# Performance work log

Measured on AMD Instinct MI355X. Metric: run time of the kernel, lower is better.

Reference implementation:

```python
import jax, jax.numpy as jnp
import numpy as np

N_NODES = 100000
N_EDGES = 1600000
IN_DIM = 128
HID = 256
N_CLS = 32
BN_EPS = 1e-5


def _sage_conv(x, src, dst, Wl, bl, Wr, n_nodes):
    # PyG SAGEConv (mean aggr): out = lin_l(mean_{j->i} x_j) + lin_r(x_i)
    msgs = x[src]                                              # [E, D] gather
    agg = jax.ops.segment_sum(msgs, dst, num_segments=n_nodes)  # [N, D]
    deg = jax.ops.segment_sum(jnp.ones((src.shape[0],), x.dtype), dst,
                              num_segments=n_nodes)
    agg = agg / jnp.maximum(deg, 1.0)[:, None]                 # mean
    return agg @ Wl + bl + x @ Wr


def _batch_norm(x, gamma, beta):
    mu = jnp.mean(x, axis=0)
    var = jnp.var(x, axis=0)
    return (x - mu) * jax.lax.rsqrt(var + BN_EPS) * gamma + beta


def setup_inputs() -> dict:
    key = jax.random.key(0)
    ks = jax.random.split(key, 8)
    s = lambda d: 1.0 / np.sqrt(d)
    return {
        "x": jax.random.normal(ks[0], (N_NODES, IN_DIM), jnp.float32),
        "edge_src": jax.random.randint(ks[1], (N_EDGES,), 0, N_NODES),
        "edge_dst": jax.random.randint(ks[2], (N_EDGES,), 0, N_NODES),
        "W1l": jax.random.normal(ks[3], (IN_DIM, HID), jnp.float32) * s(IN_DIM),
        "b1": jnp.zeros((HID,), jnp.float32),
        "W1r": jax.random.normal(ks[4], (IN_DIM, HID), jnp.float32) * s(IN_DIM),
        "g1": jnp.ones((HID,), jnp.float32),
        "be1": jnp.zeros((HID,), jnp.float32),
        "W2l": jax.random.normal(ks[5], (HID, HID), jnp.float32) * s(HID),
        "b2": jnp.zeros((HID,), jnp.float32),
        "W2r": jax.random.normal(ks[6], (HID, HID), jnp.float32) * s(HID),
        "g2": jnp.ones((HID,), jnp.float32),
        "be2": jnp.zeros((HID,), jnp.float32),
        "Wfc": jax.random.normal(ks[7], (HID, N_CLS), jnp.float32) * s(HID),
        "bfc": jnp.zeros((N_CLS,), jnp.float32),
    }


def reference(x, edge_src, edge_dst, W1l, b1, W1r, g1, be1,
              W2l, b2, W2r, g2, be2, Wfc, bfc):
    n = x.shape[0]
    h = _sage_conv(x, edge_src, edge_dst, W1l, b1, W1r, n)
    h = jax.nn.relu(_batch_norm(h, g1, be1))
    # dropout is identity in deterministic/eval mode
    h = _sage_conv(h, edge_src, edge_dst, W2l, b2, W2r, n)
    h = jax.nn.relu(_batch_norm(h, g2, be2))
    return h @ Wfc + bfc
```

## Files before the change

### kernel.cpp

```cpp
#include <hip/hip_runtime.h>

#define N_NODES 100000
#define N_EDGES 1600000
#define IN_DIM 128
#define HID 256
#define N_CLS 32
#define BN_EPS 1e-5f

#define SCAN_CHUNK 1024
#define SCAN_NB ((N_NODES + SCAN_CHUNK - 1) / SCAN_CHUNK)
#define GEMM_NBY ((N_NODES + 127) / 128)
#define GEMM_NB (GEMM_NBY * 2)

#define NBUCK 16
#define BUCK_NODES 6250
#define BUCK_CAP 112000
#define PASSA_CHUNK 2048
#define PASSA_NB ((N_EDGES + PASSA_CHUNK - 1) / PASSA_CHUNK)
#define HSUBS 32

typedef unsigned short bf16;
typedef __attribute__((ext_vector_type(8))) short short8;
typedef __attribute__((ext_vector_type(4))) float float4v;
typedef __attribute__((ext_vector_type(2))) float floatx2;

__device__ __forceinline__ float bf2f(bf16 h) {
    return __uint_as_float(((unsigned int)h) << 16);
}
__device__ __forceinline__ bf16 f2bf(float f) {
    unsigned int u = __float_as_uint(f);
    u += 0x7FFFu + ((u >> 16) & 1u);
    return (bf16)(u >> 16);
}
__device__ __forceinline__ float blo(unsigned int u) { return __uint_as_float(u << 16); }
__device__ __forceinline__ float bhi(unsigned int u) { return __uint_as_float(u & 0xFFFF0000u); }
__device__ __forceinline__ unsigned int pack2(float lo, float hi) {
    return (unsigned int)f2bf(lo) | ((unsigned int)f2bf(hi) << 16);
}

__device__ __forceinline__ void acc16_fp8(uint4 w, floatx2* a) {
    a[0] += __builtin_amdgcn_cvt_pk_f32_fp8(w.x, false);
    a[1] += __builtin_amdgcn_cvt_pk_f32_fp8(w.x, true);
    a[2] += __builtin_amdgcn_cvt_pk_f32_fp8(w.y, false);
    a[3] += __builtin_amdgcn_cvt_pk_f32_fp8(w.y, true);
    a[4] += __builtin_amdgcn_cvt_pk_f32_fp8(w.z, false);
    a[5] += __builtin_amdgcn_cvt_pk_f32_fp8(w.z, true);
    a[6] += __builtin_amdgcn_cvt_pk_f32_fp8(w.w, false);
    a[7] += __builtin_amdgcn_cvt_pk_f32_fp8(w.w, true);
}
__device__ __forceinline__ unsigned int pack4_fp8(float a, float b, float c, float d) {
    int p = 0;
    p = __builtin_amdgcn_cvt_pk_fp8_f32(a, b, p, false);
    p = __builtin_amdgcn_cvt_pk_fp8_f32(c, d, p, true);
    return (unsigned int)p;
}

__device__ __forceinline__ void gload16(const void* g, void* l) {
    __builtin_amdgcn_global_load_lds(
        (const __attribute__((address_space(1))) void*)g,
        (__attribute__((address_space(3))) void*)l, 16, 0, 0);
}


__global__ __launch_bounds__(256) void bucket_scatter_kernel(
    const int* __restrict__ esrc, const int* __restrict__ edst,
    int* __restrict__ bcur, int2* __restrict__ bstore) {
    __shared__ int lhist[NBUCK], lbase[NBUCK], gbase[NBUCK], lcur[NBUCK];
    __shared__ int2 stage[PASSA_CHUNK];
    const int tid = threadIdx.x;
    if (tid < NBUCK) lhist[tid] = 0;
    __syncthreads();

    const int base = blockIdx.x * PASSA_CHUNK;
    const int nedge = min(PASSA_CHUNK, N_EDGES - base);
    const bool act = (tid * 8) < nedge;
    int s[8], d[8], bk[8];
    if (act) {
        const int4* s4 = (const int4*)(esrc + base + tid * 8);
        const int4* d4 = (const int4*)(edst + base + tid * 8);
#pragma unroll
        for (int t = 0; t < 2; ++t) {
            int4 sv = s4[t], dv = d4[t];
            s[t * 4 + 0] = sv.x; s[t * 4 + 1] = sv.y; s[t * 4 + 2] = sv.z; s[t * 4 + 3] = sv.w;
            d[t * 4 + 0] = dv.x; d[t * 4 + 1] = dv.y; d[t * 4 + 2] = dv.z; d[t * 4 + 3] = dv.w;
        }
#pragma unroll
        for (int u = 0; u < 8; ++u) {
            bk[u] = (int)((unsigned)d[u] / BUCK_NODES);
            atomicAdd(&lhist[bk[u]], 1);
        }
    }
    __syncthreads();
    if (tid == 0) {
        int run = 0;
#pragma unroll
        for (int b = 0; b < NBUCK; ++b) { lbase[b] = run; lcur[b] = run; run += lhist[b]; }
    }
    if (tid < NBUCK) gbase[tid] = atomicAdd(&bcur[tid], lhist[tid]);
    __syncthreads();
    if (act) {
#pragma unroll
        for (int u = 0; u < 8; ++u) {
            int p = atomicAdd(&lcur[bk[u]], 1);
            stage[p] = make_int2(s[u], d[u]);
        }
    }
    __syncthreads();
    for (int p = tid; p < nedge; p += 256) {
        int2 e = stage[p];
        int b = (int)((unsigned)e.y / BUCK_NODES);
        int gp = gbase[b] + (p - lbase[b]);
        if (gp < BUCK_CAP) bstore[(size_t)b * BUCK_CAP + gp] = e;
    }
}


__global__ __launch_bounds__(256) void bucket_hist_kernel(
    const int2* __restrict__ bstore, const int* __restrict__ bcnt,
    int* __restrict__ partial) {
    __shared__ int hist[BUCK_NODES];
    const int bk = blockIdx.x & (NBUCK - 1);
    const int sl = blockIdx.x >> 4;
    for (int i = threadIdx.x; i < BUCK_NODES; i += 256) hist[i] = 0;
    __syncthreads();
    const int n = bcnt[bk];
    const int per = (n + HSUBS - 1) / HSUBS;
    const int i0 = sl * per, i1 = min(i0 + per, n);
    const int2* ep = bstore + (size_t)bk * BUCK_CAP;
    const int nbase = bk * BUCK_NODES;
    for (int i = i0 + threadIdx.x; i < i1; i += 256) {
        atomicAdd(&hist[ep[i].y - nbase], 1);
    }
    __syncthreads();
    int* dst = partial + (size_t)sl * N_NODES + nbase;
    for (int i = threadIdx.x; i < BUCK_NODES; i += 256) dst[i] = hist[i];
}


__global__ __launch_bounds__(256) void fill_bucket_kernel(
    const int2* __restrict__ bstore, const int* __restrict__ bcnt,
    const int* __restrict__ off, const int* __restrict__ partial,
    int* __restrict__ csr) {
    __shared__ int basec[BUCK_NODES];
    const int bk = blockIdx.x & (NBUCK - 1);
    const int sl = blockIdx.x >> 4;
    const int nbase = bk * BUCK_NODES;
    const int* prow = partial + (size_t)sl * N_NODES + nbase;
    const int* orow = off + nbase;
    for (int i = threadIdx.x; i < BUCK_NODES; i += 256) basec[i] = orow[i] + prow[i];
    __syncthreads();
    const int n = bcnt[bk];
    const int per = (n + HSUBS - 1) / HSUBS;
    const int i0 = sl * per, i1 = min(i0 + per, n);
    const int2* ep = bstore + (size_t)bk * BUCK_CAP;
    for (int i = i0 + threadIdx.x; i < i1; i += 256) {
        int2 e = ep[i];
        int p = atomicAdd(&basec[e.y - nbase], 1);
        csr[p] = e.x;
    }
}


__global__ void scan1_kernel(int* __restrict__ partial, int* __restrict__ counts,
                             int* __restrict__ bsums) {
    __shared__ int wsum[4];
    int base = blockIdx.x * SCAN_CHUNK + threadIdx.x * 4;
    int c0 = 0, c1 = 0, c2 = 0, c3 = 0;
    if (base + 4 <= N_NODES) {
#pragma unroll
        for (int sl = 0; sl < HSUBS; ++sl) {
            int* p = partial + (size_t)sl * N_NODES + base;
            int4 v = *(const int4*)p;
            int4 w; w.x = c0; w.y = c1; w.z = c2; w.w = c3;
            *(int4*)p = w;
            c0 += v.x; c1 += v.y; c2 += v.z; c3 += v.w;
        }
        int4 w; w.x = c0; w.y = c1; w.z = c2; w.w = c3;
        *(int4*)(counts + base) = w;
    } else {
        for (int j = 0; j < 4; ++j) {
            if (base + j < N_NODES) {
                int c = 0;
                for (int sl = 0; sl < HSUBS; ++sl) {
                    int* p = partial + (size_t)sl * N_NODES + base + j;
                    int v = *p; *p = c; c += v;
                }
                counts[base + j] = c;
                if (j == 0) c0 = c; else if (j == 1) c1 = c; else if (j == 2) c2 = c; else c3 = c;
            }
        }
    }
    int s = c0 + c1 + c2 + c3;
    for (int d = 32; d > 0; d >>= 1) s += __shfl_down(s, d, 64);
    if ((threadIdx.x & 63) == 0) wsum[threadIdx.x >> 6] = s;
    __syncthreads();
    if (threadIdx.x == 0) bsums[blockIdx.x] = wsum[0] + wsum[1] + wsum[2] + wsum[3];
}

__global__ void scan2_kernel(const int* __restrict__ bsums, int* __restrict__ boffs) {
    __shared__ int sh[128];
    int i = threadIdx.x;
    int v = (i < SCAN_NB) ? bsums[i] : 0;
    sh[i] = v;
    __syncthreads();
    for (int d = 1; d < 128; d <<= 1) {
        int t = (i >= d) ? sh[i - d] : 0;
        __syncthreads();
        sh[i] += t;
        __syncthreads();
    }
    if (i < SCAN_NB) boffs[i] = sh[i] - v;
}

__global__ void scan3_kernel(const int* __restrict__ counts, const int* __restrict__ boffs,
                             int* __restrict__ off) {
    __shared__ int sh[256];
    int tid = threadIdx.x;
    int base = blockIdx.x * SCAN_CHUNK + tid * 4;
    int c0 = 0, c1 = 0, c2 = 0, c3 = 0;
    if (base + 4 <= N_NODES) {
        int4 v = *(const int4*)(counts + base);
        c0 = v.x; c1 = v.y; c2 = v.z; c3 = v.w;
    } else {
        if (base + 0 < N_NODES) c0 = counts[base + 0];
        if (base + 1 < N_NODES) c1 = counts[base + 1];
        if (base + 2 < N_NODES) c2 = counts[base + 2];
        if (base + 3 < N_NODES) c3 = counts[base + 3];
    }
    int ts = c0 + c1 + c2 + c3;
    sh[tid] = ts;
    __syncthreads();
    for (int d = 1; d < 256; d <<= 1) {
        int t = (tid >= d) ? sh[tid - d] : 0;
        __syncthreads();
        sh[tid] += t;
        __syncthreads();
    }
    int run = boffs[blockIdx.x] + sh[tid] - ts;
    if (base + 0 < N_NODES) off[base + 0] = run; run += c0;
    if (base + 1 < N_NODES) off[base + 1] = run; run += c1;
    if (base + 2 < N_NODES) off[base + 2] = run; run += c2;
    if (base + 3 < N_NODES) off[base + 3] = run;
    if (blockIdx.x == 0 && tid == 0) off[N_NODES] = N_EDGES;
}


__global__ void convert_x_kernel(const float* __restrict__ x, bf16* __restrict__ xb,
                                 unsigned char* __restrict__ xf8) {
    int i = blockIdx.x * blockDim.x + threadIdx.x;
    int total4 = N_NODES * IN_DIM / 4;
    if (i >= total4) return;
    float4 v = ((const float4*)x)[i];
    ushort4 r;
    r.x = f2bf(v.x); r.y = f2bf(v.y); r.z = f2bf(v.z); r.w = f2bf(v.w);
    ((ushort4*)xb)[i] = r;
    ((unsigned int*)xf8)[i] = pack4_fp8(v.x, v.y, v.z, v.w);
}


__global__ void prep_weights_kernel(const float* __restrict__ W1l, const float* __restrict__ W1r,
                                    const float* __restrict__ W2l, const float* __restrict__ W2r,
                                    const float* __restrict__ Wfc,
                                    bf16* __restrict__ w1lt, bf16* __restrict__ w1rt,
                                    bf16* __restrict__ w2lt, bf16* __restrict__ w2rt,
                                    bf16* __restrict__ wfct) {
    const int S1 = IN_DIM * HID;
    const int S2 = HID * HID;
    const int S3 = HID * N_CLS;
    int i = blockIdx.x * blockDim.x + threadIdx.x;
    if (i < 2 * S1 + 2 * S2) {
        const float* W; bf16* Wt; int K, idx;
        if (i < S1)          { W = W1l; Wt = w1lt; K = IN_DIM; idx = i; }
        else if (i < 2 * S1) { W = W1r; Wt = w1rt; K = IN_DIM; idx = i - S1; }
        else if (i < 2 * S1 + S2) { W = W2l; Wt = w2lt; K = HID; idx = i - 2 * S1; }
        else                 { W = W2r; Wt = w2rt; K = HID; idx = i - 2 * S1 - S2; }
        int k = idx / HID, n = idx - k * HID;
        Wt[(size_t)n * K + k] = f2bf(W[idx]);
    } else if (i < 2 * S1 + 2 * S2 + S3) {
        int idx = i - 2 * S1 - 2 * S2;
        int k = idx >> 5, n = idx & 31;
        wfct[(size_t)n * HID + k] = f2bf(Wfc[idx]);
    }
}


__global__ __launch_bounds__(256) void aggregate1_kernel(
    const unsigned char* __restrict__ xf8, const int* __restrict__ off,
    const int* __restrict__ csr, bf16* __restrict__ out) {
    int t = blockIdx.x * blockDim.x + threadIdx.x;
    int node = t >> 3;
    int sl = t & 7;
    if (node >= N_NODES) return;
    int s = off[node], e = off[node + 1];
    float inv = 1.0f / (float)max(e - s, 1);
    const uint4* f = (const uint4*)xf8;
    floatx2 a[8];
#pragma unroll
    for (int k = 0; k < 8; ++k) a[k] = (floatx2){0.f, 0.f};
    int i = s;
    for (; i + 8 <= e; i += 8) {
        uint4 w[8];
#pragma unroll
        for (int u = 0; u < 8; ++u) w[u] = f[csr[i + u] * 8 + sl];
#pragma unroll
        for (int u = 0; u < 8; ++u) acc16_fp8(w[u], a);
    }
    for (; i + 4 <= e; i += 4) {
        uint4 w[4];
#pragma unroll
        for (int u = 0; u < 4; ++u) w[u] = f[csr[i + u] * 8 + sl];
#pragma unroll
        for (int u = 0; u < 4; ++u) acc16_fp8(w[u], a);
    }
    for (; i < e; ++i) acc16_fp8(f[csr[i] * 8 + sl], a);
    uint4 r0, r1;
    r0.x = pack2(a[0].x * inv, a[0].y * inv);
    r0.y = pack2(a[1].x * inv, a[1].y * inv);
    r0.z = pack2(a[2].x * inv, a[2].y * inv);
    r0.w = pack2(a[3].x * inv, a[3].y * inv);
    r1.x = pack2(a[4].x * inv, a[4].y * inv);
    r1.y = pack2(a[5].x * inv, a[5].y * inv);
    r1.z = pack2(a[6].x * inv, a[6].y * inv);
    r1.w = pack2(a[7].x * inv, a[7].y * inv);
    ((uint4*)out)[node * 16 + sl * 2] = r0;
    ((uint4*)out)[node * 16 + sl * 2 + 1] = r1;
}

__global__ __launch_bounds__(256) void aggregate2_kernel(
    const unsigned char* __restrict__ hf8, const int* __restrict__ off,
    const int* __restrict__ csr, bf16* __restrict__ out) {
    int t = blockIdx.x * blockDim.x + threadIdx.x;
    int node = t >> 4;
    int sl = t & 15;
    if (node >= N_NODES) return;
    int s = off[node], e = off[node + 1];
    float inv = 1.0f / (float)max(e - s, 1);
    const uint4* f = (const uint4*)hf8;
    floatx2 a[8];
#pragma unroll
    for (int k = 0; k < 8; ++k) a[k] = (floatx2){0.f, 0.f};
    int i = s;
    for (; i + 8 <= e; i += 8) {
        uint4 w[8];
#pragma unroll
        for (int u = 0; u < 8; ++u) w[u] = f[csr[i + u] * 16 + sl];
#pragma unroll
        for (int u = 0; u < 8; ++u) acc16_fp8(w[u], a);
    }
    for (; i + 4 <= e; i += 4) {
        uint4 w[4];
#pragma unroll
        for (int u = 0; u < 4; ++u) w[u] = f[csr[i + u] * 16 + sl];
#pragma unroll
        for (int u = 0; u < 4; ++u) acc16_fp8(w[u], a);
    }
    for (; i < e; ++i) acc16_fp8(f[csr[i] * 16 + sl], a);
    uint4 r0, r1;
    r0.x = pack2(a[0].x * inv, a[0].y * inv);
    r0.y = pack2(a[1].x * inv, a[1].y * inv);
    r0.z = pack2(a[2].x * inv, a[2].y * inv);
    r0.w = pack2(a[3].x * inv, a[3].y * inv);
    r1.x = pack2(a[4].x * inv, a[4].y * inv);
    r1.y = pack2(a[5].x * inv, a[5].y * inv);
    r1.z = pack2(a[6].x * inv, a[6].y * inv);
    r1.w = pack2(a[7].x * inv, a[7].y * inv);
    ((uint4*)out)[node * 32 + sl * 2] = r0;
    ((uint4*)out)[node * 32 + sl * 2 + 1] = r1;
}


#define AT_SZ 4096

__device__ __forceinline__ void stage_tile(
    const bf16* __restrict__ Ap, const bf16* __restrict__ Wp, int K, int k0,
    int tile_m, int tile_n, int M, int wave, int lane,
    bf16* bufA, bf16* bufW) {
#pragma unroll
    for (int is = 0; is < 2; ++is) {
        int lin = (wave * 2 + is) * 1024 + lane * 16;
        int row = lin >> 6;
        int seg = (lin >> 4) & 3;
        int ga = min(tile_m + row, M - 1);
        gload16(Ap + (size_t)ga * K + k0 + seg * 8, (char*)bufA + (wave * 2 + is) * 1024);
        gload16(Wp + (size_t)(tile_n + row) * K + k0 + seg * 8, (char*)bufW + (wave * 2 + is) * 1024);
    }
}

__global__ __launch_bounds__(256) void gemm_dual_mfma(
    const bf16* __restrict__ A, const bf16* __restrict__ WtA, int KA,
    const bf16* __restrict__ Bm, const bf16* __restrict__ WtB, int KB,
    const float* __restrict__ bias, bf16* __restrict__ C, int M,
    float* __restrict__ psum, float* __restrict__ psq) {
    __shared__ bf16 As[3 * AT_SZ];
    __shared__ bf16 Ws[3 * AT_SZ];
    __shared__ float sred[4][64];
    __shared__ float qred[4][64];
    const int tid = threadIdx.x;
    const int lane = tid & 63;
    const int wave = tid >> 6;
    const int rw = (wave >> 1) * 64;
    const int cw = (wave & 1) * 64;
    const int lrow = lane & 15;
    const int quad = lane >> 4;
    const int tile_m = blockIdx.y * 128;
    const int tile_n = blockIdx.x * 128;

    float4v acc[4][4];
#pragma unroll
    for (int i = 0; i < 4; ++i)
#pragma unroll
        for (int j = 0; j < 4; ++j) acc[i][j] = (float4v){0.f, 0.f, 0.f, 0.f};

    const int NTA = KA >> 5;
    const int NT = NTA + (KB >> 5);
    auto tsrc = [&](int t, const bf16*& Ap, const bf16*& Wp, int& K, int& k0) {
        if (t < NTA) { Ap = A;  Wp = WtA; K = KA; k0 = t << 5; }
        else         { Ap = Bm; Wp = WtB; K = KB; k0 = (t - NTA) << 5; }
    };

#pragma unroll
    for (int t = 0; t < 2; ++t) {
        const bf16 *Ap, *Wp; int K, k0; tsrc(t, Ap, Wp, K, k0);
        stage_tile(Ap, Wp, K, k0, tile_m, tile_n, M, wave, lane,
                   As + t * AT_SZ, Ws + t * AT_SZ);
    }

    for (int t = 0; t < NT; ++t) {
        if (t + 2 < NT) {
            const bf16 *Ap, *Wp; int K, k0; tsrc(t + 2, Ap, Wp, K, k0);
            int b = (t + 2) % 3;
            stage_tile(Ap, Wp, K, k0, tile_m, tile_n, M, wave, lane,
                       As + b * AT_SZ, Ws + b * AT_SZ);
        }
        if (t + 2 < NT)      asm volatile("s_waitcnt vmcnt(8)" ::: "memory");
        else if (t + 1 < NT) asm volatile("s_waitcnt vmcnt(4)" ::: "memory");
        else                 asm volatile("s_waitcnt vmcnt(0)" ::: "memory");
        __builtin_amdgcn_s_barrier();
        asm volatile("" ::: "memory");

        const bf16* bA = As + (t % 3) * AT_SZ;
        const bf16* bW = Ws + (t % 3) * AT_SZ;
        short8 a[4], b[4];
#pragma unroll
        for (int i = 0; i < 4; ++i)
            a[i] = *(const short8*)(bA + (rw + i * 16 + lrow) * 32 + quad * 8);
#pragma unroll
        for (int j = 0; j < 4; ++j)
            b[j] = *(const short8*)(bW + (cw + j * 16 + lrow) * 32 + quad * 8);
#pragma unroll
        for (int i = 0; i < 4; ++i)
#pragma unroll
            for (int j = 0; j < 4; ++j)
                acc[i][j] = __builtin_amdgcn_mfma_f32_16x16x32_bf16(a[i], b[j], acc[i][j], 0, 0, 0);

        asm volatile("" ::: "memory");
        __builtin_amdgcn_s_barrier();
    }

    bf16* slice = As + wave * 1024;
    float bvj[4];
#pragma unroll
    for (int j = 0; j < 4; ++j) bvj[j] = bias[tile_n + cw + j * 16 + lrow];
    float cs[4] = {0.f, 0.f, 0.f, 0.f}, cq[4] = {0.f, 0.f, 0.f, 0.f};

#pragma unroll
    for (int i = 0; i < 4; ++i) {
#pragma unroll
        for (int j = 0; j < 4; ++j) {
#pragma unroll
            for (int r = 0; r < 4; ++r) {
                int row = tile_m + rw + i * 16 + quad * 4 + r;
                float v = acc[i][j][r] + bvj[j];
                if (row < M) { cs[j] += v; cq[j] += v * v; }
                slice[(quad * 4 + r) * 64 + ((j ^ quad) * 16) + lrow] = f2bf(v);
            }
        }
        __syncthreads();
#pragma unroll
        for (int c = 0; c < 2; ++c) {
            int ch = lane + c * 64;
            int lr = ch >> 3, sg = ch & 7;
            int grow = tile_m + rw + i * 16 + lr;
            if (grow < M) {
                const bf16* srcp = slice + lr * 64 + (((sg >> 1) ^ (lr >> 2)) << 4) + ((sg & 1) << 3);
                uint4 v = *(const uint4*)srcp;
                *(uint4*)(C + (size_t)grow * HID + tile_n + cw + sg * 8) = v;
            }
        }
        __syncthreads();
    }

#pragma unroll
    for (int j = 0; j < 4; ++j) {
        cs[j] += __shfl_xor(cs[j], 16, 64); cs[j] += __shfl_xor(cs[j], 32, 64);
        cq[j] += __shfl_xor(cq[j], 16, 64); cq[j] += __shfl_xor(cq[j], 32, 64);
    }
    if (quad == 0) {
#pragma unroll
        for (int j = 0; j < 4; ++j) {
            sred[wave][j * 16 + lrow] = cs[j];
            qred[wave][j * 16 + lrow] = cq[j];
        }
    }
    __syncthreads();
    int bid = blockIdx.y * gridDim.x + blockIdx.x;
    if (tid < 128) {
        int grp = tid >> 6, idx = tid & 63;
        psum[(size_t)bid * 128 + tid] = sred[grp][idx] + sred[grp + 2][idx];
    } else {
        int t = tid - 128;
        int grp = t >> 6, idx = t & 63;
        psq[(size_t)bid * 128 + t] = qred[grp][idx] + qred[grp + 2][idx];
    }
}

__global__ void bn_finalize_kernel(const float* __restrict__ psum, const float* __restrict__ psq,
                                   float* __restrict__ stats, int nby) {
    const float* src = blockIdx.y ? psq : psum;
    int c = threadIdx.x;
    int bx = c >> 7, cl = c & 127;
    int per = (nby + gridDim.x - 1) / gridDim.x;
    int b0 = blockIdx.x * per, b1 = min(b0 + per, nby);
    float s = 0.f;
    for (int by = b0; by < b1; ++by) s += src[(size_t)(by * 2 + bx) * 128 + cl];
    atomicAdd(&stats[blockIdx.y * HID + c], s);
}


__global__ void bn_apply_relu_kernel(bf16* __restrict__ h, unsigned char* __restrict__ hf8,
                                     const float* __restrict__ stats,
                                     const float* __restrict__ g, const float* __restrict__ be,
                                     int M) {
    int i4 = blockIdx.x * blockDim.x + threadIdx.x;
    int total4 = M * (HID / 4);
    if (i4 >= total4) return;
    int col4 = i4 & (HID / 4 - 1);
    ushort4 v = ((const ushort4*)h)[i4];
    float invN = 1.0f / (float)M;
    float o[4] = {bf2f(v.x), bf2f(v.y), bf2f(v.z), bf2f(v.w)};
#pragma unroll
    for (int j = 0; j < 4; ++j) {
        int col = col4 * 4 + j;
        float mu = stats[col] * invN;
        float var = stats[HID + col] * invN - mu * mu;
        float sc = rsqrtf(var + BN_EPS) * g[col];
        float val = (o[j] - mu) * sc + be[col];
        o[j] = val > 0.f ? val : 0.f;
    }
    ushort4 r;
    r.x = f2bf(o[0]); r.y = f2bf(o[1]); r.z = f2bf(o[2]); r.w = f2bf(o[3]);
    ((ushort4*)h)[i4] = r;
    ((unsigned int*)hf8)[i4] = pack4_fp8(o[0], o[1], o[2], o[3]);
}


#define BSTR 264

__global__ __launch_bounds__(256) void fc_bn_mfma_kernel(
    const bf16* __restrict__ h, const float* __restrict__ stats,
    const float* __restrict__ g, const float* __restrict__ be,
    const bf16* __restrict__ WfcT, const float* __restrict__ bfc,
    float* __restrict__ out, int M) {
    __shared__ bf16 Bs[32 * BSTR];
    __shared__ float sc_s[HID], sh_s[HID];
    int tid = threadIdx.x;
    for (int i = tid; i < 32 * 32; i += 256) {
        int rrow = i >> 5, seg = i & 31;
        *(uint4*)(Bs + rrow * BSTR + seg * 8) = *(const uint4*)(WfcT + (size_t)rrow * HID + seg * 8);
    }
    {
        float invN = 1.0f / (float)M;
        float mu = stats[tid] * invN;
        float var = stats[HID + tid] * invN - mu * mu;
        float s = rsqrtf(var + BN_EPS) * g[tid];
        sc_s[tid] = s;
        sh_s[tid] = be[tid] - mu * s;
    }
    __syncthreads();
    int wave = tid >> 6, lane = tid & 63, lrow = lane & 15, quad = lane >> 4;
    int row = blockIdx.x * 64 + wave * 16 + lrow;
    const bf16* hrow = h + (size_t)row * HID;
    float4v acc0 = {0.f, 0.f, 0.f, 0.f}, acc1 = {0.f, 0.f, 0.f, 0.f};
#pragma unroll
    for (int ks = 0; ks < 8; ++ks) {
        int k0 = ks * 32 + quad * 8;
        uint4 av = {0u, 0u, 0u, 0u};
        if (row < M) av = *(const uint4*)(hrow + k0);
        union { unsigned int u[4]; short8 s8; } cvt;
        unsigned int* avp = (unsigned int*)&av;
#pragma unroll
        for (int t = 0; t < 4; ++t) {
            int k = k0 + t * 2;
            float v0 = blo(avp[t]) * sc_s[k] + sh_s[k];
            float v1 = bhi(avp[t]) * sc_s[k + 1] + sh_s[k + 1];
            v0 = v0 > 0.f ? v0 : 0.f;
            v1 = v1 > 0.f ? v1 : 0.f;
            cvt.u[t] = pack2(v0, v1);
        }
        short8 b0 = *(const short8*)(Bs + lrow * BSTR + k0);
        short8 b1 = *(const short8*)(Bs + (16 + lrow) * BSTR + k0);
        acc0 = __builtin_amdgcn_mfma_f32_16x16x32_bf16(cvt.s8, b0, acc0, 0, 0, 0);
        acc1 = __builtin_amdgcn_mfma_f32_16x16x32_bf16(cvt.s8, b1, acc1, 0, 0, 0);
    }
    int orow = blockIdx.x * 64 + wave * 16 + quad * 4;
    float bv0 = bfc[lrow], bv1 = bfc[16 + lrow];
#pragma unroll
    for (int r = 0; r < 4; ++r) {
        int rr = orow + r;
        if (rr < M) {
            out[(size_t)rr * N_CLS + lrow] = acc0[r] + bv0;
            out[(size_t)rr * N_CLS + 16 + lrow] = acc1[r] + bv1;
        }
    }
}


extern "C" void kernel_launch(void* const* d_in, const int* in_sizes, int n_in,
                              void* d_out, int out_size, void* d_ws, size_t ws_size,
                              hipStream_t stream) {
    const float* x   = (const float*)d_in[0];
    const int* esrc  = (const int*)d_in[1];
    const int* edst  = (const int*)d_in[2];
    const float* W1l = (const float*)d_in[3];
    const float* b1  = (const float*)d_in[4];
    const float* W1r = (const float*)d_in[5];
    const float* g1  = (const float*)d_in[6];
    const float* be1 = (const float*)d_in[7];
    const float* W2l = (const float*)d_in[8];
    const float* b2  = (const float*)d_in[9];
    const float* W2r = (const float*)d_in[10];
    const float* g2  = (const float*)d_in[11];
    const float* be2 = (const float*)d_in[12];
    const float* Wfc = (const float*)d_in[13];
    const float* bfc = (const float*)d_in[14];
    float* out = (float*)d_out;

    char* ws = (char*)d_ws;
    size_t o = 0;
    auto carve = [&](size_t bytes) {
        char* p = ws + o;
        o = (o + bytes + 255) & ~(size_t)255;
        return p;
    };
    int*   off    = (int*)carve((N_NODES + 1) * sizeof(int));
    int*   cursor = (int*)carve(N_NODES * sizeof(int));
    int*   csr    = (int*)carve(N_EDGES * sizeof(int));
    int*   bsums  = (int*)carve(SCAN_NB * sizeof(int));
    int*   boffs  = (int*)carve(SCAN_NB * sizeof(int));
    int*   bcur   = (int*)carve(NBUCK * sizeof(int));
    float* stats1 = (float*)carve(2 * HID * sizeof(float));
    float* stats2 = (float*)carve(2 * HID * sizeof(float));
    float* psum   = (float*)carve((size_t)GEMM_NB * 128 * sizeof(float));
    float* psq    = (float*)carve((size_t)GEMM_NB * 128 * sizeof(float));
    bf16*  w1lt   = (bf16*)carve((size_t)IN_DIM * HID * sizeof(bf16));
    bf16*  w1rt   = (bf16*)carve((size_t)IN_DIM * HID * sizeof(bf16));
    bf16*  w2lt   = (bf16*)carve((size_t)HID * HID * sizeof(bf16));
    bf16*  w2rt   = (bf16*)carve((size_t)HID * HID * sizeof(bf16));
    bf16*  wfct   = (bf16*)carve((size_t)N_CLS * HID * sizeof(bf16));
    bf16*  agg    = (bf16*)carve((size_t)N_NODES * HID * sizeof(bf16));
    bf16*  h1     = (bf16*)carve((size_t)N_NODES * HID * sizeof(bf16));
    bf16*  h2     = (bf16*)carve((size_t)N_NODES * HID * sizeof(bf16));
    bf16*          xb   = h2;
    unsigned char* xf8  = (unsigned char*)h2 + (size_t)N_NODES * IN_DIM * sizeof(bf16);
    unsigned char* h1f8 = (unsigned char*)h2;
    int2*          bstore = (int2*)agg;
    int*           partial = (int*)h1;

    if (o > ws_size) return;

    hipMemsetAsync(bcur, 0, NBUCK * sizeof(int), stream);
    hipMemsetAsync(stats1, 0, 2 * HID * sizeof(float), stream);
    hipMemsetAsync(stats2, 0, 2 * HID * sizeof(float), stream);

    bucket_scatter_kernel<<<PASSA_NB, 256, 0, stream>>>(esrc, edst, bcur, bstore);
    bucket_hist_kernel<<<NBUCK * HSUBS, 256, 0, stream>>>(bstore, bcur, partial);
    scan1_kernel<<<SCAN_NB, 256, 0, stream>>>(partial, cursor, bsums);
    scan2_kernel<<<1, 128, 0, stream>>>(bsums, boffs);
    scan3_kernel<<<SCAN_NB, 256, 0, stream>>>(cursor, boffs, off);
    fill_bucket_kernel<<<NBUCK * HSUBS, 256, 0, stream>>>(bstore, bcur, off, partial, csr);

    convert_x_kernel<<<(N_NODES * IN_DIM / 4 + 255) / 256, 256, 0, stream>>>(x, xb, xf8);
    {
        int total = 2 * IN_DIM * HID + 2 * HID * HID + HID * N_CLS;
        prep_weights_kernel<<<(total + 255) / 256, 256, 0, stream>>>(
            W1l, W1r, W2l, W2r, Wfc, w1lt, w1rt, w2lt, w2rt, wfct);
    }

    const dim3 ggrid(HID / 128, GEMM_NBY);

    aggregate1_kernel<<<(N_NODES * 8 + 255) / 256, 256, 0, stream>>>(xf8, off, csr, agg);
    gemm_dual_mfma<<<ggrid, 256, 0, stream>>>(
        agg, w1lt, IN_DIM, xb, w1rt, IN_DIM, b1, h1, N_NODES, psum, psq);
    bn_finalize_kernel<<<dim3(8, 2), 256, 0, stream>>>(psum, psq, stats1, GEMM_NBY);
    {
        int total4 = N_NODES * (HID / 4);
        bn_apply_relu_kernel<<<(total4 + 255) / 256, 256, 0, stream>>>(h1, h1f8, stats1, g1, be1, N_NODES);
    }

    aggregate2_kernel<<<(N_NODES * 16 + 255) / 256, 256, 0, stream>>>(h1f8, off, csr, agg);
    gemm_dual_mfma<<<ggrid, 256, 0, stream>>>(
        agg, w2lt, HID, h1, w2rt, HID, b2, h2, N_NODES, psum, psq);
    bn_finalize_kernel<<<dim3(8, 2), 256, 0, stream>>>(psum, psq, stats2, GEMM_NBY);

    fc_bn_mfma_kernel<<<(N_NODES + 63) / 64, 256, 0, stream>>>(
        h2, stats2, g2, be2, wfct, bfc, out, N_NODES);
}
```

Before: 454.1 us.

## Remap aggregation threads to feature slices across blocks, add nontemporal csr/output access

Aggregation kernels now assign each block one 32-byte feature slice for a range of nodes, two threads per node, with adjacent block IDs covering different slices of the same nodes. Previously all slices of a node were handled by consecutive threads of one wavefront. The aim is to narrow the gather working set per block so it fits cache better, and to keep concurrent blocks touching nearby rows. The csr index loads and the aggregated output stores are made nontemporal so they do not evict cached feature rows. In exchange, each block reads csr and offsets separately for every slice, repeating index traffic and divergent degree loops.

```diff
diff --git a/kernel.cpp b/kernel.cpp
--- a/kernel.cpp
+++ b/kernel.cpp
@@ -23,6 +23,7 @@
 typedef __attribute__((ext_vector_type(8))) short short8;
 typedef __attribute__((ext_vector_type(4))) float float4v;
 typedef __attribute__((ext_vector_type(2))) float floatx2;
+typedef __attribute__((ext_vector_type(4))) unsigned int uint4v;
 
 __device__ __forceinline__ float bf2f(bf16 h) {
     return __uint_as_float(((unsigned int)h) << 16);
@@ -287,13 +288,15 @@
 __global__ __launch_bounds__(256) void aggregate1_kernel(
     const unsigned char* __restrict__ xf8, const int* __restrict__ off,
     const int* __restrict__ csr, bf16* __restrict__ out) {
-    int t = blockIdx.x * blockDim.x + threadIdx.x;
-    int node = t >> 3;
-    int sl = t & 7;
+    const int key = blockIdx.x & 7;
+    const int slice = key >> 1;
+    const int node = (blockIdx.x >> 3) * 256 + (key & 1) * 128 + (threadIdx.x >> 1);
+    const int half = threadIdx.x & 1;
     if (node >= N_NODES) return;
     int s = off[node], e = off[node + 1];
     float inv = 1.0f / (float)max(e - s, 1);
     const uint4* f = (const uint4*)xf8;
+    const int boff = slice * 2 + half;
     floatx2 a[8];
 #pragma unroll
     for (int k = 0; k < 8; ++k) a[k] = (floatx2){0.f, 0.f};
@@ -301,19 +304,19 @@
     for (; i + 8 <= e; i += 8) {
         uint4 w[8];
 #pragma unroll
-        for (int u = 0; u < 8; ++u) w[u] = f[csr[i + u] * 8 + sl];
+        for (int u = 0; u < 8; ++u) w[u] = f[__builtin_nontemporal_load(csr + i + u) * 8 + boff];
 #pragma unroll
         for (int u = 0; u < 8; ++u) acc16_fp8(w[u], a);
     }
     for (; i + 4 <= e; i += 4) {
         uint4 w[4];
 #pragma unroll
-        for (int u = 0; u < 4; ++u) w[u] = f[csr[i + u] * 8 + sl];
+        for (int u = 0; u < 4; ++u) w[u] = f[__builtin_nontemporal_load(csr + i + u) * 8 + boff];
 #pragma unroll
         for (int u = 0; u < 4; ++u) acc16_fp8(w[u], a);
     }
-    for (; i < e; ++i) acc16_fp8(f[csr[i] * 8 + sl], a);
-    uint4 r0, r1;
+    for (; i < e; ++i) acc16_fp8(f[__builtin_nontemporal_load(csr + i) * 8 + boff], a);
+    uint4v r0, r1;
     r0.x = pack2(a[0].x * inv, a[0].y * inv);
     r0.y = pack2(a[1].x * inv, a[1].y * inv);
     r0.z = pack2(a[2].x * inv, a[2].y * inv);
@@ -322,20 +325,22 @@
     r1.y = pack2(a[5].x * inv, a[5].y * inv);
     r1.z = pack2(a[6].x * inv, a[6].y * inv);
     r1.w = pack2(a[7].x * inv, a[7].y * inv);
-    ((uint4*)out)[node * 16 + sl * 2] = r0;
-    ((uint4*)out)[node * 16 + sl * 2 + 1] = r1;
+    uint4v* dst = (uint4v*)out + node * 16 + slice * 4 + half * 2;
+    __builtin_nontemporal_store(r0, dst);
+    __builtin_nontemporal_store(r1, dst + 1);
 }
 
 __global__ __launch_bounds__(256) void aggregate2_kernel(
     const unsigned char* __restrict__ hf8, const int* __restrict__ off,
     const int* __restrict__ csr, bf16* __restrict__ out) {
-    int t = blockIdx.x * blockDim.x + threadIdx.x;
-    int node = t >> 4;
-    int sl = t & 15;
+    const int slice = blockIdx.x & 7;
+    const int node = (blockIdx.x >> 3) * 128 + (threadIdx.x >> 1);
+    const int half = threadIdx.x & 1;
     if (node >= N_NODES) return;
     int s = off[node], e = off[node + 1];
     float inv = 1.0f / (float)max(e - s, 1);
     const uint4* f = (const uint4*)hf8;
+    const int boff = slice * 2 + half;
     floatx2 a[8];
 #pragma unroll
     for (int k = 0; k < 8; ++k) a[k] = (floatx2){0.f, 0.f};
@@ -343,19 +348,19 @@
     for (; i + 8 <= e; i += 8) {
         uint4 w[8];
 #pragma unroll
-        for (int u = 0; u < 8; ++u) w[u] = f[csr[i + u] * 16 + sl];
+        for (int u = 0; u < 8; ++u) w[u] = f[__builtin_nontemporal_load(csr + i + u) * 16 + boff];
 #pragma unroll
         for (int u = 0; u < 8; ++u) acc16_fp8(w[u], a);
     }
     for (; i + 4 <= e; i += 4) {
         uint4 w[4];
 #pragma unroll
-        for (int u = 0; u < 4; ++u) w[u] = f[csr[i + u] * 16 + sl];
+        for (int u = 0; u < 4; ++u) w[u] = f[__builtin_nontemporal_load(csr + i + u) * 16 + boff];
 #pragma unroll
         for (int u = 0; u < 4; ++u) acc16_fp8(w[u], a);
     }
-    for (; i < e; ++i) acc16_fp8(f[csr[i] * 16 + sl], a);
-    uint4 r0, r1;
+    for (; i < e; ++i) acc16_fp8(f[__builtin_nontemporal_load(csr + i) * 16 + boff], a);
+    uint4v r0, r1;
     r0.x = pack2(a[0].x * inv, a[0].y * inv);
     r0.y = pack2(a[1].x * inv, a[1].y * inv);
     r0.z = pack2(a[2].x * inv, a[2].y * inv);
@@ -364,8 +369,9 @@
     r1.y = pack2(a[5].x * inv, a[5].y * inv);
     r1.z = pack2(a[6].x * inv, a[6].y * inv);
     r1.w = pack2(a[7].x * inv, a[7].y * inv);
-    ((uint4*)out)[node * 32 + sl * 2] = r0;
-    ((uint4*)out)[node * 32 + sl * 2 + 1] = r1;
+    uint4v* dst = (uint4v*)out + node * 32 + slice * 4 + half * 2;
+    __builtin_nontemporal_store(r0, dst);
+    __builtin_nontemporal_store(r1, dst + 1);
 }
 
 
@@ -688,7 +694,7 @@
 
     const dim3 ggrid(HID / 128, GEMM_NBY);
 
-    aggregate1_kernel<<<(N_NODES * 8 + 255) / 256, 256, 0, stream>>>(xf8, off, csr, agg);
+    aggregate1_kernel<<<8 * ((N_NODES + 255) / 256), 256, 0, stream>>>(xf8, off, csr, agg);
     gemm_dual_mfma<<<ggrid, 256, 0, stream>>>(
         agg, w1lt, IN_DIM, xb, w1rt, IN_DIM, b1, h1, N_NODES, psum, psq);
     bn_finalize_kernel<<<dim3(8, 2), 256, 0, stream>>>(psum, psq, stats1, GEMM_NBY);
@@ -697,7 +703,7 @@
         bn_apply_relu_kernel<<<(total4 + 255) / 256, 256, 0, stream>>>(h1, h1f8, stats1, g1, be1, N_NODES);
     }
 
-    aggregate2_kernel<<<(N_NODES * 16 + 255) / 256, 256, 0, stream>>>(h1f8, off, csr, agg);
+    aggregate2_kernel<<<8 * ((N_NODES + 127) / 128), 256, 0, stream>>>(h1f8, off, csr, agg);
     gemm_dual_mfma<<<ggrid, 256, 0, stream>>>(
         agg, w2lt, HID, h1, w2rt, HID, b2, h2, N_NODES, psum, psq);
     bn_finalize_kernel<<<dim3(8, 2), 256, 0, stream>>>(psum, psq, stats2, GEMM_NBY);
```

New measurement: 676.3 us. 48.9% more time.
